# Kernel tuning notes

Measured on AMD Instinct MI355X. Metric: run time of the kernel, lower is better.

## Reference

```python
import jax, jax.numpy as jnp
import numpy as np

B, T, N, D = 4, 24, 5000, 64
M, K = 256, 20
TEMP = 0.5
MASK_T = int(T * 0.2)


def _random_walk(A):
    # D^-1 A with inf -> 0, as in calculate_random_walk_matrix
    deg = A.sum(axis=1)
    d_inv = jnp.where(deg > 0, 1.0 / deg, 0.0)
    return d_inv[:, None] * A


def _gnn(h, S1, S2, W, b):
    # SpatialConvOrderK, order=1, support_len=2, include_self=True
    # h: [B, C, N, T]; diffusion along node axis; 1x1 conv == channel matmul
    m1 = jnp.einsum('bcnt,mn->bcmt', h, S1)
    m2 = jnp.einsum('bcnt,mn->bcmt', h, S2)
    hc = jnp.concatenate([h, m1, m2], axis=1)  # [B, 3C, N, T]
    return jnp.einsum('bcnt,cd->bdnt', hc, W) + b[None, :, None, None]


def _encode(x, S1, S2, W_start, b_start, W1, b1, W2, b2):
    h = x @ W_start + b_start                 # [B, T, N, D]
    h = jnp.transpose(h, (0, 3, 2, 1))        # [B, D, N, T]
    h = jax.nn.relu(_gnn(h, S1, S2, W1, b1))
    h = _gnn(h, S1, S2, W2, b2)
    return h                                  # [B, D, N, T]


def _normalize(z):
    # cosine-similarity normalization over channel axis (dim=1), torch eps=1e-8
    n = jnp.sqrt(jnp.sum(z * z, axis=1, keepdims=True))
    return z / jnp.maximum(n, 1e-8)


def _forward(x, adj, W_start, b_start, W1, b1, W2, b2, Wf1, bf1, Wf2, bf2,
             missing_idx, pos_idx, neg_idx):
    S1 = _random_walk(adj)
    S2 = _random_walk(adj.T)
    h_ori = _encode(x, S1, S2, W_start, b_start, W1, b1, W2, b2)
    # augmented view: time-masked input through the same encoder
    x_aug = x.at[:, :MASK_T].set(0.0)
    h_aug = _encode(x_aug, S1, S2, W_start, b_start, W1, b1, W2, b2)
    # imputation head: final_linear1 -> relu -> final_linear2
    ht = jnp.transpose(h_ori, (0, 3, 2, 1))   # [B, T, N, D]
    y = jax.nn.relu(ht @ Wf1 + bf1) @ Wf2 + bf2  # [B, T, N, 1]
    # vectorized RSCL: batched gather + cosine sim + InfoNCE (label 0 = positive)
    Zo = _normalize(jnp.transpose(h_ori, (0, 1, 3, 2)))  # [B, D, T, N]
    Za = _normalize(jnp.transpose(h_aug, (0, 1, 3, 2)))
    anchor = Zo[..., missing_idx]             # [B, D, T, M]
    pos = Za[..., pos_idx]                    # [B, D, T, M]
    neg = Za[..., neg_idx]                    # [B, D, T, M, K]
    pos_sim = jnp.sum(anchor * pos, axis=1)                  # [B, T, M]
    neg_sim = jnp.einsum('bdtm,bdtmk->btmk', anchor, neg)    # [B, T, M, K]
    logits = jnp.concatenate([pos_sim[..., None], neg_sim], axis=-1) / TEMP
    # cross-entropy with label 0 == logsumexp - positive logit
    loss = jnp.mean(jax.nn.logsumexp(logits, axis=-1) - logits[..., 0])
    return y, loss


def setup_inputs() -> dict:
    key = jax.random.key(0)
    ks = jax.random.split(key, 12)
    x = jax.random.normal(ks[0], (B, T, N, 1), jnp.float32)
    adj = jax.random.uniform(ks[1], (N, N), jnp.float32)
    missing_idx = jax.random.randint(ks[2], (M,), 0, N)
    pos_idx = jax.random.randint(ks[3], (M,), 0, N)
    neg_idx = jax.random.randint(ks[4], (M, K), 0, N)
    s = lambda k, shp, fan: (jax.random.normal(k, shp, jnp.float32) / np.sqrt(fan)).astype(jnp.float32)
    W_start = s(ks[5], (1, D), 1.0)
    b_start = jnp.zeros((D,), jnp.float32)
    W1 = s(ks[6], (3 * D, D), 3.0 * D)
    b1 = jnp.zeros((D,), jnp.float32)
    W2 = s(ks[7], (3 * D, D), 3.0 * D)
    b2 = jnp.zeros((D,), jnp.float32)
    Wf1 = s(ks[8], (D, D // 2), float(D))
    bf1 = jnp.zeros((D // 2,), jnp.float32)
    Wf2 = s(ks[9], (D // 2, 1), float(D // 2))
    bf2 = jnp.zeros((1,), jnp.float32)
    return dict(x=x, adj=adj, W_start=W_start, b_start=b_start, W1=W1, b1=b1,
                W2=W2, b2=b2, Wf1=Wf1, bf1=bf1, Wf2=Wf2, bf2=bf2,
                missing_idx=missing_idx, pos_idx=pos_idx, neg_idx=neg_idx)


def reference(x, adj, W_start, b_start, W1, b1, W2, b2, Wf1, bf1, Wf2, bf2,
              missing_idx, pos_idx, neg_idx):
    return _forward(x, adj, W_start, b_start, W1, b1, W2, b2, Wf1, bf1, Wf2, bf2,
                    missing_idx, pos_idx, neg_idx)
```

## Files before the change

### kernel.cpp

```cpp
#include <hip/hip_runtime.h>

typedef unsigned char u8;
typedef unsigned short u16;
typedef unsigned int u32;
typedef __attribute__((ext_vector_type(8))) short short8;
typedef __attribute__((ext_vector_type(8))) u16 u16x8;
typedef __attribute__((ext_vector_type(4))) float f32x4;
typedef __attribute__((ext_vector_type(4))) int i32x4;
typedef __attribute__((ext_vector_type(8))) int i32x8;

#define N_NODES 5000
#define NP 5120
#define BTOT 96
#define J_DIM 6144
#define TT 24
#define KNEG 20

__device__ __forceinline__ float b2f(u16 u){ union{u32 i; float f;} x; x.i = ((u32)u)<<16; return x.f; }
__device__ __forceinline__ u16 f2b(float f){ union{float fl; u32 i;} x; x.fl = f; u32 r = (x.i + 0x7fffu + ((x.i>>16)&1u))>>16; return (u16)r; }
__device__ __forceinline__ u8 f2e4(float f){ return (u8)(__builtin_amdgcn_cvt_pk_fp8_f32(f, 0.f, 0, false) & 0xff); }

#define GPERM(r) ((((r)>>1)&3) | (((r)&1)<<2))
#define GLOAD16(g, l) __builtin_amdgcn_global_load_lds((const __attribute__((address_space(1))) void*)(g), (__attribute__((address_space(3))) void*)(l), 16, 0, 0)

__global__ void k_prep(const float* __restrict__ Ws, const float* __restrict__ bs,
                       const float* __restrict__ W1, const float* __restrict__ b1,
                       const float* __restrict__ W2, const float* __restrict__ b2,
                       float* __restrict__ consts, u16* __restrict__ w2t)
{
  int d = threadIdx.x;
  float u0=0.f,u1=0.f,u2=0.f,bb=0.f;
  for (int c=0;c<64;c++){
    float w = Ws[c];
    float a = W1[c*64+d], b_ = W1[(64+c)*64+d], cw = W1[(128+c)*64+d];
    u0 += w*a; u1 += w*b_; u2 += w*cw;
    bb += bs[c]*(a+b_+cw);
  }
  bb += b1[d];
  consts[d]=u0; consts[64+d]=u1; consts[128+d]=u2; consts[192+d]=bb;
  __shared__ float rb[64];
  rb[d] = fmaxf(bb, 0.f);
  __syncthreads();
  float cA=0.f,cB=0.f,cC=0.f;
  for (int c=0;c<64;c++){
    float r = rb[c];
    cA += r*W2[c*64+d]; cB += r*W2[(64+c)*64+d]; cC += r*W2[(128+c)*64+d];
  }
  consts[256+d]=cA; consts[320+d]=cB; consts[384+d]=cC;
  for (int c=0;c<192;c++) w2t[d*192 + c] = f2b(W2[c*64 + d]);
  __syncthreads();
  float b2v = b2[d];
  for (int vi=0; vi<4; vi++){
    float vv = cA + ((vi&1) ? cB : 0.f) + ((vi&2) ? cC : 0.f) + b2v;
    rb[d] = vv*vv;
    __syncthreads();
    for (int o=32;o;o>>=1){ if (d<o) rb[d]+=rb[d+o]; __syncthreads(); }
    float nrm = sqrtf(rb[0]);
    consts[448 + vi*64 + d] = vv / fmaxf(nrm, 1e-8f);
    __syncthreads();
  }
}

__global__ __launch_bounds__(256) void k_convT(const float* __restrict__ adj,
    u8* __restrict__ abf, u8* __restrict__ atbf,
    float* __restrict__ degr, float* __restrict__ degc)
{
  __shared__ u8 tN[64][80];
  __shared__ u8 tT[64][80];
  __shared__ float rsum[64];
  __shared__ float cpart[16][64];
  const int tid = threadIdx.x;
  const int bx = blockIdx.x, by = blockIdx.y;
  const int c4 = (tid & 15) * 4;
  const int g  = tid >> 4;
  const int gk = bx*64 + c4;
  float ca0=0.f, ca1=0.f, ca2=0.f, ca3=0.f;
  #pragma unroll
  for (int p=0;p<4;p++){
    int r = p*16 + g;
    int gm = by*64 + r;
    float v0=0.f,v1=0.f,v2=0.f,v3=0.f;
    if (gm < N_NODES && gk + 3 < N_NODES){
      const float4 v = *(const float4*)(adj + (size_t)gm*N_NODES + gk);
      v0=v.x; v1=v.y; v2=v.z; v3=v.w;
    }
    u8 p0=f2e4(v0), p1=f2e4(v1), p2=f2e4(v2), p3=f2e4(v3);
    *(u32*)&tN[r][c4] = (u32)p0 | ((u32)p1<<8) | ((u32)p2<<16) | ((u32)p3<<24);
    tT[c4+0][r]=p0; tT[c4+1][r]=p1; tT[c4+2][r]=p2; tT[c4+3][r]=p3;
    float ls = v0+v1+v2+v3;
    ls += __shfl_xor(ls,1); ls += __shfl_xor(ls,2);
    ls += __shfl_xor(ls,4); ls += __shfl_xor(ls,8);
    if ((tid & 15) == 0) rsum[r] = ls;
    ca0+=v0; ca1+=v1; ca2+=v2; ca3+=v3;
  }
  cpart[g][c4+0]=ca0; cpart[g][c4+1]=ca1; cpart[g][c4+2]=ca2; cpart[g][c4+3]=ca3;
  __syncthreads();
  if (tid < 64){
    int gm = by*64 + tid;
    if (gm < N_NODES && rsum[tid] != 0.f) atomicAdd(&degr[gm], rsum[tid]);
    float cs = 0.f;
    #pragma unroll
    for (int gg=0;gg<16;gg++) cs += cpart[gg][tid];
    int gc = bx*64 + tid;
    if (gc < N_NODES && cs != 0.f) atomicAdd(&degc[gc], cs);
  }
  const int j = tid >> 2, c16 = (tid & 3) * 16;
  *(i32x4*)(abf  + (size_t)(by*64+j)*NP + bx*64 + c16) = *(const i32x4*)(&tN[j][c16]);
  *(i32x4*)(atbf + (size_t)(bx*64+j)*NP + by*64 + c16) = *(const i32x4*)(&tT[j][c16]);
}

__global__ void k_xbf(const float* __restrict__ x, u8* __restrict__ xbf){
  int i4 = (blockIdx.x*256 + threadIdx.x)*4;
  int j = i4 / NP, n = i4 - j*NP;
  u32 w = 0;
  if (j < BTOT){
    #pragma unroll
    for (int e=0;e<4;e++){
      float v = (n+e < N_NODES) ? x[(size_t)j*N_NODES + n + e] : 0.f;
      w |= ((u32)f2e4(v)) << (8*e);
    }
  }
  *(u32*)(xbf + i4) = w;
}

__device__ __forceinline__ i32x8 frag8(const u8* lds, int row, int kb2){
  int g = GPERM(row & 7);
  int ba = row*128 + ((kb2 ^ g)<<4);
  union { i32x8 v; i32x4 h[2]; } f;
  f.h[0] = *(const i32x4*)(lds + ba);
  f.h[1] = *(const i32x4*)(lds + (ba^16));
  return f.v;
}

__global__ __launch_bounds__(256) void k_sgemm8(const u8* __restrict__ abf,
    const u8* __restrict__ atbf, const u8* __restrict__ B,
    float* __restrict__ y1sl, float* __restrict__ y2sl)
{
  __shared__ __align__(16) u8 lA[128*128];
  __shared__ __align__(16) u8 lB[128*128];
  const u8* A = blockIdx.z ? atbf : abf;
  float* ysl = blockIdx.z ? y2sl : y1sl;
  const int tid = threadIdx.x, lane = tid & 63, wv = tid >> 6;
  const int wm = (wv >> 1) * 64, wj = (wv & 1) * 64;
  const int m0 = blockIdx.x * 128;
  const int kbase = blockIdx.y * 640;
  f32x4 acc[4][4] = {};
  const int q = tid >> 3;
  const int sc = ((tid & 7) ^ GPERM(q & 7)) << 4;
  const u8* gA = A + (size_t)(m0 + q)*NP + kbase + sc;
  const u8* gB = B + (size_t)q*NP + kbase + sc;
  for (int k0 = 0; k0 < 640; k0 += 128) {
    #pragma unroll
    for (int s=0;s<4;s++){
      GLOAD16(gA + (size_t)(s*32)*NP + k0, (char*)lA + s*4096 + wv*1024);
      GLOAD16(gB + (size_t)(s*32)*NP + k0, (char*)lB + s*4096 + wv*1024);
    }
    __syncthreads();
    i32x8 af[4], bfv[4];
    const int kb2 = (lane >> 4) * 2;
    #pragma unroll
    for (int i=0;i<4;i++){
      af[i]  = frag8(lA, wm + i*16 + (lane&15), kb2);
      bfv[i] = frag8(lB, wj + i*16 + (lane&15), kb2);
    }
    #pragma unroll
    for (int i=0;i<4;i++)
      #pragma unroll
      for (int j=0;j<4;j++)
        acc[i][j] = __builtin_amdgcn_mfma_scale_f32_16x16x128_f8f6f4(
            af[i], bfv[j], acc[i][j], 0, 0, 0, 0x7f7f7f7f, 0, 0x7f7f7f7f);
    __syncthreads();
  }
  float* yb = ysl + (size_t)blockIdx.y * NP * 128;
  #pragma unroll
  for (int i=0;i<4;i++)
    #pragma unroll
    for (int r=0;r<4;r++){
      int row = m0 + wm + i*16 + (lane>>4)*4 + r;
      #pragma unroll
      for (int j=0;j<4;j++){
        int col = wj + j*16 + (lane&15);
        yb[(size_t)row*128 + col] = acc[i][j][r];
      }
    }
}

__global__ __launch_bounds__(256) void k_yred(const float* __restrict__ y1sl,
    const float* __restrict__ y2sl, const float* __restrict__ degr,
    const float* __restrict__ degc, float* __restrict__ y1r, float* __restrict__ y2r)
{
  __shared__ float tb[128][66];
  const int n0 = blockIdx.x*64;
  const int bt = threadIdx.x & 127, nh = threadIdx.x >> 7;
  const int nl = threadIdx.x & 63, bh = threadIdx.x >> 6;
  #pragma unroll 4
  for (int k=0;k<32;k++){
    int n = nh*32 + k;
    float s = 0.f;
    #pragma unroll
    for (int sl=0; sl<8; sl++) s += y1sl[((size_t)sl*NP + n0+n)*128 + bt];
    tb[bt][n] = s;
  }
  __syncthreads();
  {
    float dv = degr[n0+nl];
    float iv = (dv > 0.f) ? 1.f/dv : 0.f;
    #pragma unroll 4
    for (int b=0;b<32;b++){
      int btw = bh*32 + b;
      y1r[(size_t)btw*NP + n0 + nl] = iv * tb[btw][nl];
    }
  }
  __syncthreads();
  #pragma unroll 4
  for (int k=0;k<32;k++){
    int n = nh*32 + k;
    float s = 0.f;
    #pragma unroll
    for (int sl=0; sl<8; sl++) s += y2sl[((size_t)sl*NP + n0+n)*128 + bt];
    tb[bt][n] = s;
  }
  __syncthreads();
  {
    float dv = degc[n0+nl];
    float iv = (dv > 0.f) ? 1.f/dv : 0.f;
    #pragma unroll 4
    for (int b=0;b<32;b++){
      int btw = bh*32 + b;
      y2r[(size_t)btw*NP + n0 + nl] = iv * tb[btw][nl];
    }
  }
}

__global__ __launch_bounds__(256) void k_h1(const float* __restrict__ x,
    const float* __restrict__ y1r, const float* __restrict__ y2r,
    const float* __restrict__ consts, u8* __restrict__ h1t, u16* __restrict__ h1n)
{
  __shared__ u8 trT[64][80];
  const int tid = threadIdx.x;
  const int n = tid & 63, d0 = (tid >> 6) * 16;
  const int n0 = blockIdx.x * 64;
  const int bt = blockIdx.y;
  const int gn = n0 + n;
  const bool valid = gn < N_NODES;
  float xv  = valid ? x[(size_t)bt*N_NODES + gn] : 0.f;
  float y1s = y1r[(size_t)bt*NP + gn];
  float y2s = y2r[(size_t)bt*NP + gn];
  float hv[16];
  #pragma unroll
  for (int e=0;e<16;e++){
    int d = d0 + e;
    float v = 0.f;
    if (valid)
      v = fmaxf(xv*consts[d] + y1s*consts[64+d] + y2s*consts[128+d] + consts[192+d], 0.f);
    hv[e] = v;
    trT[d][n] = f2e4(v);
  }
  u16x8 p0, p1;
  #pragma unroll
  for (int e=0;e<8;e++){ p0[e]=f2b(hv[e]); p1[e]=f2b(hv[8+e]); }
  u16* dst = h1n + (size_t)gn*J_DIM + bt*64 + d0;
  *(u16x8*)dst = p0;
  *(u16x8*)(dst+8) = p1;
  __syncthreads();
  const int d = tid >> 2, c16 = (tid & 3) * 16;
  *(i32x4*)(h1t + (size_t)(bt*64+d)*NP + n0 + c16) = *(const i32x4*)(&trT[d][c16]);
}

__global__ __launch_bounds__(256) void k_gemm8(
    const u8* __restrict__ abf, const u8* __restrict__ atbf,
    const u8* __restrict__ Bt, u16* __restrict__ Pb, u16* __restrict__ Qb,
    const float* __restrict__ degr, const float* __restrict__ degc)
{
  __shared__ __align__(16) u8 lA[2][16384];
  __shared__ __align__(16) u8 lB[2][16384];
  const u8* A = blockIdx.z ? atbf : abf;
  u16* C = blockIdx.z ? Qb : Pb;
  const float* dg = blockIdx.z ? degc : degr;
  const int tid = threadIdx.x, lane = tid & 63, wv = tid >> 6;
  const int wm = (wv >> 1) * 64, wj = (wv & 1) * 64;
  const int m0 = blockIdx.x * 128;
  const int j0 = blockIdx.y * 128;
  f32x4 acc[4][4] = {};
  const int q = tid >> 3;
  const int sc = ((tid & 7) ^ GPERM(q & 7)) << 4;
  const u8* gA = A + (size_t)(m0 + q)*NP + sc;
  const u8* gB = Bt + (size_t)(j0 + q)*NP + sc;

  #define STAGE8(k0, bufA, bufB) do { \
    _Pragma("unroll") \
    for (int s=0;s<4;s++){ \
      GLOAD16(gA + (size_t)(s*32)*NP + (k0), (char*)(bufA) + s*4096 + wv*1024); \
      GLOAD16(gB + (size_t)(s*32)*NP + (k0), (char*)(bufB) + s*4096 + wv*1024); \
    } \
  } while(0)

  STAGE8(0,   lA[0], lB[0]);
  STAGE8(128, lA[1], lB[1]);
  asm volatile("s_waitcnt vmcnt(8)" ::: "memory");
  __builtin_amdgcn_s_barrier();
  __builtin_amdgcn_sched_barrier(0);

  const int NT = NP/128;
  for (int t = 0; t < NT; t++) {
    const int cur = t & 1;
    const u8* bA = lA[cur];
    const u8* bB = lB[cur];
    i32x8 af[4], bfv[4];
    const int kb2 = (lane >> 4) * 2;
    #pragma unroll
    for (int i=0;i<4;i++){
      af[i]  = frag8(bA, wm + i*16 + (lane&15), kb2);
      bfv[i] = frag8(bB, wj + i*16 + (lane&15), kb2);
    }
    __builtin_amdgcn_s_setprio(1);
    #pragma unroll
    for (int i=0;i<4;i++)
      #pragma unroll
      for (int j=0;j<4;j++)
        acc[i][j] = __builtin_amdgcn_mfma_scale_f32_16x16x128_f8f6f4(
            af[i], bfv[j], acc[i][j], 0, 0, 0, 0x7f7f7f7f, 0, 0x7f7f7f7f);
    __builtin_amdgcn_s_setprio(0);
    __builtin_amdgcn_s_barrier();
    __builtin_amdgcn_sched_barrier(0);
    if (t + 2 < NT) {
      STAGE8((t+2)*128, lA[cur], lB[cur]);
      asm volatile("s_waitcnt vmcnt(8)" ::: "memory");
    } else {
      asm volatile("s_waitcnt vmcnt(0)" ::: "memory");
    }
    __builtin_amdgcn_s_barrier();
    __builtin_amdgcn_sched_barrier(0);
  }
  #undef STAGE8

  #pragma unroll
  for (int i=0;i<4;i++)
    #pragma unroll
    for (int r=0;r<4;r++){
      int row = m0 + wm + i*16 + (lane>>4)*4 + r;
      float dv = dg[row];
      float scl = (dv > 0.f) ? 1.f/dv : 0.f;
      #pragma unroll
      for (int j=0;j<4;j++){
        int col = j0 + wj + j*16 + (lane&15);
        C[(size_t)row*J_DIM + col] = f2b(acc[i][j][r] * scl);
      }
    }
}

__global__ __launch_bounds__(256) void k_comb(const u16* __restrict__ h1n,
  const u16* __restrict__ P, const u16* __restrict__ Q,
  const u16* __restrict__ w2t, const float* __restrict__ b2,
  const float* __restrict__ Wf1, const float* __restrict__ bf1,
  const float* __restrict__ Wf2, const float* __restrict__ bf2,
  u16* __restrict__ horin, float* __restrict__ yout)
{
  __shared__ float w1L[64*33];
  __shared__ float hT[64][65];
  __shared__ float b1L[32], w2Ls[32];
  const int tid = threadIdx.x;
  for (int i = tid; i < 2048; i += 256) w1L[(i>>5)*33 + (i&31)] = Wf1[i];
  if (tid < 32){ b1L[tid] = bf1[tid]; w2Ls[tid] = Wf2[tid]; }
  const int lane = tid & 63;
  const int wv = tid >> 6;
  const int n0 = blockIdx.x * 64 + wv * 16;
  const int bt = blockIdx.y;
  const int rl = lane & 15, kh = lane >> 4;

  f32x4 acc[4] = {};
  const size_t rowoff = (size_t)(n0 + rl) * J_DIM + bt*64;
  const u16* bases[3] = { h1n + rowoff, P + rowoff, Q + rowoff };
  #pragma unroll
  for (int s=0;s<3;s++){
    const u16* base = bases[s];
    #pragma unroll
    for (int kk=0;kk<2;kk++){
      short8 af = *(const short8*)(base + kk*32 + kh*8);
      #pragma unroll
      for (int j=0;j<4;j++){
        short8 bf = *(const short8*)(w2t + (j*16+rl)*192 + s*64 + kk*32 + kh*8);
        acc[j] = __builtin_amdgcn_mfma_f32_16x16x32_bf16(af, bf, acc[j], 0,0,0);
      }
    }
  }
  float hvv[4][4];
  #pragma unroll
  for (int j=0;j<4;j++){
    float bias = b2[j*16 + rl];
    #pragma unroll
    for (int r=0;r<4;r++) hvv[j][r] = acc[j][r] + bias;
  }
  float inv[4];
  #pragma unroll
  for (int r=0;r<4;r++){
    float s = hvv[0][r]*hvv[0][r] + hvv[1][r]*hvv[1][r]
            + hvv[2][r]*hvv[2][r] + hvv[3][r]*hvv[3][r];
    s += __shfl_xor(s,1); s += __shfl_xor(s,2);
    s += __shfl_xor(s,4); s += __shfl_xor(s,8);
    inv[r] = 1.f / fmaxf(sqrtf(s), 1e-8f);
  }
  #pragma unroll
  for (int j=0;j<4;j++){
    int d = j*16 + rl;
    #pragma unroll
    for (int r=0;r<4;r++){
      int nn = n0 + kh*4 + r;
      hT[wv*16 + kh*4 + r][d] = hvv[j][r];
      if (nn < N_NODES)
        horin[((size_t)bt*N_NODES + nn)*64 + d] = f2b(hvv[j][r] * inv[r]);
    }
  }
  __syncthreads();
  const int qd = tid & 3, node = tid >> 2;
  float h[16];
  #pragma unroll
  for (int e=0;e<16;e++) h[e] = hT[node][qd*16 + e];
  float yacc = 0.f;
  #pragma unroll
  for (int jj=0; jj<32; jj++){
    float s = 0.f;
    #pragma unroll
    for (int dl=0; dl<16; dl++) s += h[dl]*w1L[(qd*16+dl)*33 + jj];
    s += __shfl_xor(s, 1);
    s += __shfl_xor(s, 2);
    s += b1L[jj];
    yacc += fmaxf(s, 0.f)*w2Ls[jj];
  }
  int gn = blockIdx.x*64 + node;
  if (qd == 0 && gn < N_NODES)
    yout[(size_t)bt*N_NODES + gn] = yacc + bf2[0];
}

__global__ __launch_bounds__(256) void k_loss(const u16* __restrict__ horin,
  const int* __restrict__ missing, const int* __restrict__ posi, const int* __restrict__ negi,
  const float* __restrict__ degr, const float* __restrict__ degc,
  const float* __restrict__ consts, float* __restrict__ out)
{
  const int lane = threadIdx.x & 63;
  const int wv = threadIdx.x >> 6;
  const int wg = blockIdx.x*4 + wv;
  const int m = wg & 255;
  const int bt = wg >> 8;
  const bool early = (bt % TT) < 4;

  int na = missing[m];
  float va = b2f(horin[((size_t)bt*N_NODES + na)*64 + lane]);

  float lk[KNEG+1];
  #pragma unroll
  for (int k=0;k<=KNEG;k++){
    int node = (k==0) ? posi[m] : negi[m*KNEG + (k-1)];
    float v;
    if (!early) v = b2f(horin[((size_t)bt*N_NODES + node)*64 + lane]);
    else {
      int vi = (degr[node] > 0.f ? 1 : 0) + (degc[node] > 0.f ? 2 : 0);
      v = consts[448 + vi*64 + lane];
    }
    float dp = va*v;
    #pragma unroll
    for (int o=32;o;o>>=1) dp += __shfl_xor(dp, o);
    lk[k] = dp * 2.f;
  }
  float mx = lk[0];
  #pragma unroll
  for (int k=1;k<=KNEG;k++) mx = fmaxf(mx, lk[k]);
  float se = 0.f;
  #pragma unroll
  for (int k=0;k<=KNEG;k++) se += expf(lk[k]-mx);
  float term = logf(se) + mx - lk[0];
  __shared__ float red[4];
  if (lane == 0) red[wv] = term;
  __syncthreads();
  if (threadIdx.x == 0)
    atomicAdd(out + 480000, (red[0]+red[1]+red[2]+red[3]) * (1.f/24576.f));
}

extern "C" void kernel_launch(void* const* d_in, const int* in_sizes, int n_in,
                              void* d_out, int out_size, void* d_ws, size_t ws_size,
                              hipStream_t stream)
{
  const float* x   = (const float*)d_in[0];
  const float* adj = (const float*)d_in[1];
  const float* Ws  = (const float*)d_in[2];
  const float* bs  = (const float*)d_in[3];
  const float* W1  = (const float*)d_in[4];
  const float* b1  = (const float*)d_in[5];
  const float* W2  = (const float*)d_in[6];
  const float* b2  = (const float*)d_in[7];
  const float* Wf1 = (const float*)d_in[8];
  const float* bf1 = (const float*)d_in[9];
  const float* Wf2 = (const float*)d_in[10];
  const float* bf2 = (const float*)d_in[11];
  const int* missing = (const int*)d_in[12];
  const int* posi    = (const int*)d_in[13];
  const int* negi    = (const int*)d_in[14];
  float* out = (float*)d_out;

  char* w = (char*)d_ws;
  u8*  abf   = (u8*) (w + 0);
  u8*  atbf  = (u8*) (w + 26214400);
  u8*  h1t   = (u8*) (w + 52428800);
  u16* h1n   = (u16*)(w + 83886080);
  u16* Pb    = (u16*)(w + 146800640);
  u16* Qb    = (u16*)(w + 209715200);
  u8*  xbf   = (u8*) (w + 272629760);
  float* degr = (float*)(w + 273285120);
  float* degc = (float*)(w + 273305600);
  float* consts = (float*)(w + 273326080);
  u16* w2t   = (u16*)(w + 273330176);
  u16*   horin = (u16*)(w + 0);
  float* y1sl  = (float*)(w + 146800640);
  float* y2sl  = (float*)(w + 167772160);
  float* y1r   = (float*)(w + 209715200);
  float* y2r   = (float*)(w + 212336640);

  hipMemsetAsync(degr, 0, 40960, stream);
  hipMemsetAsync(out + 480000, 0, 4, stream);

  k_prep<<<1, 64, 0, stream>>>(Ws, bs, W1, b1, W2, b2, consts, w2t);
  k_convT<<<dim3(80,80), 256, 0, stream>>>(adj, abf, atbf, degr, degc);
  k_xbf<<<640, 256, 0, stream>>>(x, xbf);
  k_sgemm8<<<dim3(40,8,2), 256, 0, stream>>>(abf, atbf, xbf, y1sl, y2sl);
  k_yred<<<80, 256, 0, stream>>>(y1sl, y2sl, degr, degc, y1r, y2r);
  k_h1<<<dim3(80,96), 256, 0, stream>>>(x, y1r, y2r, consts, h1t, h1n);
  k_gemm8<<<dim3(40,48,2), 256, 0, stream>>>(abf, atbf, h1t, Pb, Qb, degr, degc);
  k_comb<<<dim3(80,96), 256, 0, stream>>>(h1n, Pb, Qb, w2t, b2, Wf1, bf1, Wf2, bf2, horin, out);
  k_loss<<<6144, 256, 0, stream>>>(horin, missing, posi, negi, degr, degc, consts, out);
}
```

Measured before the change: 672.3 us.

## Store diffusion outputs P/Q as fp8 and double-buffer the small fp8 GEMM

```diff
diff --git a/kernel.cpp b/kernel.cpp
--- a/kernel.cpp
+++ b/kernel.cpp
@@ -19,6 +19,23 @@
 __device__ __forceinline__ float b2f(u16 u){ union{u32 i; float f;} x; x.i = ((u32)u)<<16; return x.f; }
 __device__ __forceinline__ u16 f2b(float f){ union{float fl; u32 i;} x; x.fl = f; u32 r = (x.i + 0x7fffu + ((x.i>>16)&1u))>>16; return (u16)r; }
 __device__ __forceinline__ u8 f2e4(float f){ return (u8)(__builtin_amdgcn_cvt_pk_fp8_f32(f, 0.f, 0, false) & 0xff); }
+__device__ __forceinline__ float e4tof(u8 v){
+  u32 s = ((u32)(v & 0x80)) << 24;
+  u32 em = v & 0x7f;
+  union{u32 i; float f;} x;
+  if (em >= 8) x.i = s | ((em + 0x3C0u) << 20);
+  else { x.f = (float)em * 0.001953125f; x.i |= s; }
+  return x.f;
+}
+__device__ __forceinline__ short8 cvt8(u32 w0, u32 w1){
+  short8 r;
+  #pragma unroll
+  for (int e=0;e<4;e++){
+    r[e]   = (short)f2b(e4tof((u8)(w0 >> (8*e))));
+    r[4+e] = (short)f2b(e4tof((u8)(w1 >> (8*e))));
+  }
+  return r;
+}
 
 #define GPERM(r) ((((r)>>1)&3) | (((r)&1)<<2))
 #define GLOAD16(g, l) __builtin_amdgcn_global_load_lds((const __attribute__((address_space(1))) void*)(g), (__attribute__((address_space(3))) void*)(l), 16, 0, 0)
@@ -136,8 +153,8 @@
     const u8* __restrict__ atbf, const u8* __restrict__ B,
     float* __restrict__ y1sl, float* __restrict__ y2sl)
 {
-  __shared__ __align__(16) u8 lA[128*128];
-  __shared__ __align__(16) u8 lB[128*128];
+  __shared__ __align__(16) u8 lA[2][16384];
+  __shared__ __align__(16) u8 lB[2][16384];
   const u8* A = blockIdx.z ? atbf : abf;
   float* ysl = blockIdx.z ? y2sl : y1sl;
   const int tid = threadIdx.x, lane = tid & 63, wv = tid >> 6;
@@ -149,28 +166,53 @@
   const int sc = ((tid & 7) ^ GPERM(q & 7)) << 4;
   const u8* gA = A + (size_t)(m0 + q)*NP + kbase + sc;
   const u8* gB = B + (size_t)q*NP + kbase + sc;
-  for (int k0 = 0; k0 < 640; k0 += 128) {
-    #pragma unroll
-    for (int s=0;s<4;s++){
-      GLOAD16(gA + (size_t)(s*32)*NP + k0, (char*)lA + s*4096 + wv*1024);
-      GLOAD16(gB + (size_t)(s*32)*NP + k0, (char*)lB + s*4096 + wv*1024);
-    }
-    __syncthreads();
+
+  #define SSTAGE8(k0, bufA, bufB) do { \
+    _Pragma("unroll") \
+    for (int s=0;s<4;s++){ \
+      GLOAD16(gA + (size_t)(s*32)*NP + (k0), (char*)(bufA) + s*4096 + wv*1024); \
+      GLOAD16(gB + (size_t)(s*32)*NP + (k0), (char*)(bufB) + s*4096 + wv*1024); \
+    } \
+  } while(0)
+
+  SSTAGE8(0,   lA[0], lB[0]);
+  SSTAGE8(128, lA[1], lB[1]);
+  asm volatile("s_waitcnt vmcnt(8)" ::: "memory");
+  __builtin_amdgcn_s_barrier();
+  __builtin_amdgcn_sched_barrier(0);
+
+  for (int t = 0; t < 5; t++) {
+    const int cur = t & 1;
+    const u8* bA = lA[cur];
+    const u8* bB = lB[cur];
     i32x8 af[4], bfv[4];
     const int kb2 = (lane >> 4) * 2;
     #pragma unroll
     for (int i=0;i<4;i++){
-      af[i]  = frag8(lA, wm + i*16 + (lane&15), kb2);
-      bfv[i] = frag8(lB, wj + i*16 + (lane&15), kb2);
-    }
+      af[i]  = frag8(bA, wm + i*16 + (lane&15), kb2);
+      bfv[i] = frag8(bB, wj + i*16 + (lane&15), kb2);
+    }
+    __builtin_amdgcn_s_setprio(1);
     #pragma unroll
     for (int i=0;i<4;i++)
       #pragma unroll
       for (int j=0;j<4;j++)
         acc[i][j] = __builtin_amdgcn_mfma_scale_f32_16x16x128_f8f6f4(
             af[i], bfv[j], acc[i][j], 0, 0, 0, 0x7f7f7f7f, 0, 0x7f7f7f7f);
-    __syncthreads();
-  }
+    __builtin_amdgcn_s_setprio(0);
+    __builtin_amdgcn_s_barrier();
+    __builtin_amdgcn_sched_barrier(0);
+    if (t + 2 < 5) {
+      SSTAGE8((t+2)*128, lA[cur], lB[cur]);
+      asm volatile("s_waitcnt vmcnt(8)" ::: "memory");
+    } else {
+      asm volatile("s_waitcnt vmcnt(0)" ::: "memory");
+    }
+    __builtin_amdgcn_s_barrier();
+    __builtin_amdgcn_sched_barrier(0);
+  }
+  #undef SSTAGE8
+
   float* yb = ysl + (size_t)blockIdx.y * NP * 128;
   #pragma unroll
   for (int i=0;i<4;i++)
@@ -269,13 +311,13 @@
 
 __global__ __launch_bounds__(256) void k_gemm8(
     const u8* __restrict__ abf, const u8* __restrict__ atbf,
-    const u8* __restrict__ Bt, u16* __restrict__ Pb, u16* __restrict__ Qb,
+    const u8* __restrict__ Bt, u8* __restrict__ Pb, u8* __restrict__ Qb,
     const float* __restrict__ degr, const float* __restrict__ degc)
 {
   __shared__ __align__(16) u8 lA[2][16384];
   __shared__ __align__(16) u8 lB[2][16384];
   const u8* A = blockIdx.z ? atbf : abf;
-  u16* C = blockIdx.z ? Qb : Pb;
+  u8* C = blockIdx.z ? Qb : Pb;
   const float* dg = blockIdx.z ? degc : degr;
   const int tid = threadIdx.x, lane = tid & 63, wv = tid >> 6;
   const int wm = (wv >> 1) * 64, wj = (wv & 1) * 64;
@@ -344,13 +386,13 @@
       #pragma unroll
       for (int j=0;j<4;j++){
         int col = j0 + wj + j*16 + (lane&15);
-        C[(size_t)row*J_DIM + col] = f2b(acc[i][j][r] * scl);
+        C[(size_t)row*J_DIM + col] = f2e4(acc[i][j][r] * scl);
       }
     }
 }
 
 __global__ __launch_bounds__(256) void k_comb(const u16* __restrict__ h1n,
-  const u16* __restrict__ P, const u16* __restrict__ Q,
+  const u8* __restrict__ P8, const u8* __restrict__ Q8,
   const u16* __restrict__ w2t, const float* __restrict__ b2,
   const float* __restrict__ Wf1, const float* __restrict__ bf1,
   const float* __restrict__ Wf2, const float* __restrict__ bf2,
@@ -369,17 +411,31 @@
   const int rl = lane & 15, kh = lane >> 4;
 
   f32x4 acc[4] = {};
-  const size_t rowoff = (size_t)(n0 + rl) * J_DIM + bt*64;
-  const u16* bases[3] = { h1n + rowoff, P + rowoff, Q + rowoff };
-  #pragma unroll
-  for (int s=0;s<3;s++){
-    const u16* base = bases[s];
+  {
+    const u16* base = h1n + (size_t)(n0 + rl)*J_DIM + bt*64;
     #pragma unroll
     for (int kk=0;kk<2;kk++){
       short8 af = *(const short8*)(base + kk*32 + kh*8);
       #pragma unroll
       for (int j=0;j<4;j++){
-        short8 bf = *(const short8*)(w2t + (j*16+rl)*192 + s*64 + kk*32 + kh*8);
+        short8 bf = *(const short8*)(w2t + (j*16+rl)*192 + kk*32 + kh*8);
+        acc[j] = __builtin_amdgcn_mfma_f32_16x16x32_bf16(af, bf, acc[j], 0,0,0);
+      }
+    }
+  }
+  const size_t rowoff8 = (size_t)(n0 + rl) * J_DIM + bt*64;
+  const u8* bases8[2] = { P8 + rowoff8, Q8 + rowoff8 };
+  #pragma unroll
+  for (int s=0;s<2;s++){
+    const u8* base = bases8[s];
+    #pragma unroll
+    for (int kk=0;kk<2;kk++){
+      u32 w0 = *(const u32*)(base + kk*32 + kh*8);
+      u32 w1 = *(const u32*)(base + kk*32 + kh*8 + 4);
+      short8 af = cvt8(w0, w1);
+      #pragma unroll
+      for (int j=0;j<4;j++){
+        short8 bf = *(const short8*)(w2t + (j*16+rl)*192 + (s+1)*64 + kk*32 + kh*8);
         acc[j] = __builtin_amdgcn_mfma_f32_16x16x32_bf16(af, bf, acc[j], 0,0,0);
       }
     }
@@ -502,18 +558,18 @@
   u8*  atbf  = (u8*) (w + 26214400);
   u8*  h1t   = (u8*) (w + 52428800);
   u16* h1n   = (u16*)(w + 83886080);
-  u16* Pb    = (u16*)(w + 146800640);
-  u16* Qb    = (u16*)(w + 209715200);
-  u8*  xbf   = (u8*) (w + 272629760);
-  float* degr = (float*)(w + 273285120);
-  float* degc = (float*)(w + 273305600);
-  float* consts = (float*)(w + 273326080);
-  u16* w2t   = (u16*)(w + 273330176);
-  u16*   horin = (u16*)(w + 0);
-  float* y1sl  = (float*)(w + 146800640);
-  float* y2sl  = (float*)(w + 167772160);
-  float* y1r   = (float*)(w + 209715200);
-  float* y2r   = (float*)(w + 212336640);
+  u8*  Pb    = (u8*) (w + 146800640);
+  u8*  Qb    = (u8*) (w + 178257920);
+  float* y1sl = (float*)(w + 209715200);
+  float* y2sl = (float*)(w + 230686720);
+  float* y1r  = (float*)(w + 251658240);
+  float* y2r  = (float*)(w + 254279680);
+  u8*  xbf   = (u8*) (w + 256901120);
+  float* degr = (float*)(w + 257556480);
+  float* degc = (float*)(w + 257576960);
+  float* consts = (float*)(w + 257597440);
+  u16* w2t   = (u16*)(w + 257601536);
+  u16* horin = (u16*)(w + 0);
 
   hipMemsetAsync(degr, 0, 40960, stream);
   hipMemsetAsync(out + 480000, 0, 4, stream);
```

Result: slower. 691.6 us (+2.9%).

## Enlarge diffusion GEMM tile to 256x256 and double-buffer the slice GEMM

Applied to the files above, without the earlier changes.

```diff
diff --git a/kernel.cpp b/kernel.cpp
--- a/kernel.cpp
+++ b/kernel.cpp
@@ -136,8 +136,8 @@
     const u8* __restrict__ atbf, const u8* __restrict__ B,
     float* __restrict__ y1sl, float* __restrict__ y2sl)
 {
-  __shared__ __align__(16) u8 lA[128*128];
-  __shared__ __align__(16) u8 lB[128*128];
+  __shared__ __align__(16) u8 lA[2][16384];
+  __shared__ __align__(16) u8 lB[2][16384];
   const u8* A = blockIdx.z ? atbf : abf;
   float* ysl = blockIdx.z ? y2sl : y1sl;
   const int tid = threadIdx.x, lane = tid & 63, wv = tid >> 6;
@@ -149,28 +149,53 @@
   const int sc = ((tid & 7) ^ GPERM(q & 7)) << 4;
   const u8* gA = A + (size_t)(m0 + q)*NP + kbase + sc;
   const u8* gB = B + (size_t)q*NP + kbase + sc;
-  for (int k0 = 0; k0 < 640; k0 += 128) {
-    #pragma unroll
-    for (int s=0;s<4;s++){
-      GLOAD16(gA + (size_t)(s*32)*NP + k0, (char*)lA + s*4096 + wv*1024);
-      GLOAD16(gB + (size_t)(s*32)*NP + k0, (char*)lB + s*4096 + wv*1024);
-    }
-    __syncthreads();
+
+  #define SSTAGE8(k0, bufA, bufB) do { \
+    _Pragma("unroll") \
+    for (int s=0;s<4;s++){ \
+      GLOAD16(gA + (size_t)(s*32)*NP + (k0), (char*)(bufA) + s*4096 + wv*1024); \
+      GLOAD16(gB + (size_t)(s*32)*NP + (k0), (char*)(bufB) + s*4096 + wv*1024); \
+    } \
+  } while(0)
+
+  SSTAGE8(0,   lA[0], lB[0]);
+  SSTAGE8(128, lA[1], lB[1]);
+  asm volatile("s_waitcnt vmcnt(8)" ::: "memory");
+  __builtin_amdgcn_s_barrier();
+  __builtin_amdgcn_sched_barrier(0);
+
+  for (int t = 0; t < 5; t++) {
+    const int cur = t & 1;
+    const u8* bA = lA[cur];
+    const u8* bB = lB[cur];
     i32x8 af[4], bfv[4];
     const int kb2 = (lane >> 4) * 2;
     #pragma unroll
     for (int i=0;i<4;i++){
-      af[i]  = frag8(lA, wm + i*16 + (lane&15), kb2);
-      bfv[i] = frag8(lB, wj + i*16 + (lane&15), kb2);
-    }
+      af[i]  = frag8(bA, wm + i*16 + (lane&15), kb2);
+      bfv[i] = frag8(bB, wj + i*16 + (lane&15), kb2);
+    }
+    __builtin_amdgcn_s_setprio(1);
     #pragma unroll
     for (int i=0;i<4;i++)
       #pragma unroll
       for (int j=0;j<4;j++)
         acc[i][j] = __builtin_amdgcn_mfma_scale_f32_16x16x128_f8f6f4(
             af[i], bfv[j], acc[i][j], 0, 0, 0, 0x7f7f7f7f, 0, 0x7f7f7f7f);
-    __syncthreads();
-  }
+    __builtin_amdgcn_s_setprio(0);
+    __builtin_amdgcn_s_barrier();
+    __builtin_amdgcn_sched_barrier(0);
+    if (t + 2 < 5) {
+      SSTAGE8((t+2)*128, lA[cur], lB[cur]);
+      asm volatile("s_waitcnt vmcnt(8)" ::: "memory");
+    } else {
+      asm volatile("s_waitcnt vmcnt(0)" ::: "memory");
+    }
+    __builtin_amdgcn_s_barrier();
+    __builtin_amdgcn_sched_barrier(0);
+  }
+  #undef SSTAGE8
+
   float* yb = ysl + (size_t)blockIdx.y * NP * 128;
   #pragma unroll
   for (int i=0;i<4;i++)
@@ -267,21 +292,22 @@
   *(i32x4*)(h1t + (size_t)(bt*64+d)*NP + n0 + c16) = *(const i32x4*)(&trT[d][c16]);
 }
 
-__global__ __launch_bounds__(256) void k_gemm8(
+__global__ __launch_bounds__(512, 2) void k_gemm8(
     const u8* __restrict__ abf, const u8* __restrict__ atbf,
     const u8* __restrict__ Bt, u16* __restrict__ Pb, u16* __restrict__ Qb,
     const float* __restrict__ degr, const float* __restrict__ degc)
 {
-  __shared__ __align__(16) u8 lA[2][16384];
-  __shared__ __align__(16) u8 lB[2][16384];
+  __shared__ __align__(16) u8 lA[2][32768];
+  __shared__ __align__(16) u8 lB[2][32768];
   const u8* A = blockIdx.z ? atbf : abf;
   u16* C = blockIdx.z ? Qb : Pb;
   const float* dg = blockIdx.z ? degc : degr;
   const int tid = threadIdx.x, lane = tid & 63, wv = tid >> 6;
-  const int wm = (wv >> 1) * 64, wj = (wv & 1) * 64;
-  const int m0 = blockIdx.x * 128;
-  const int j0 = blockIdx.y * 128;
-  f32x4 acc[4][4] = {};
+  const int wm = (wv >> 1) * 64;
+  const int wn = (wv & 1) * 128;
+  const int m0 = blockIdx.x * 256;
+  const int j0 = blockIdx.y * 256;
+  f32x4 acc[4][8] = {};
   const int q = tid >> 3;
   const int sc = ((tid & 7) ^ GPERM(q & 7)) << 4;
   const u8* gA = A + (size_t)(m0 + q)*NP + sc;
@@ -290,8 +316,8 @@
   #define STAGE8(k0, bufA, bufB) do { \
     _Pragma("unroll") \
     for (int s=0;s<4;s++){ \
-      GLOAD16(gA + (size_t)(s*32)*NP + (k0), (char*)(bufA) + s*4096 + wv*1024); \
-      GLOAD16(gB + (size_t)(s*32)*NP + (k0), (char*)(bufB) + s*4096 + wv*1024); \
+      GLOAD16(gA + (size_t)(s*64)*NP + (k0), (char*)(bufA) + s*8192 + wv*1024); \
+      GLOAD16(gB + (size_t)(s*64)*NP + (k0), (char*)(bufB) + s*8192 + wv*1024); \
     } \
   } while(0)
 
@@ -306,20 +332,20 @@
     const int cur = t & 1;
     const u8* bA = lA[cur];
     const u8* bB = lB[cur];
-    i32x8 af[4], bfv[4];
     const int kb2 = (lane >> 4) * 2;
-    #pragma unroll
-    for (int i=0;i<4;i++){
-      af[i]  = frag8(bA, wm + i*16 + (lane&15), kb2);
-      bfv[i] = frag8(bB, wj + i*16 + (lane&15), kb2);
-    }
+    const int rl = lane & 15;
+    i32x8 af[4];
+    #pragma unroll
+    for (int i=0;i<4;i++) af[i] = frag8(bA, wm + i*16 + rl, kb2);
     __builtin_amdgcn_s_setprio(1);
     #pragma unroll
-    for (int i=0;i<4;i++)
+    for (int j=0;j<8;j++){
+      i32x8 bf = frag8(bB, wn + j*16 + rl, kb2);
       #pragma unroll
-      for (int j=0;j<4;j++)
+      for (int i=0;i<4;i++)
         acc[i][j] = __builtin_amdgcn_mfma_scale_f32_16x16x128_f8f6f4(
-            af[i], bfv[j], acc[i][j], 0, 0, 0, 0x7f7f7f7f, 0, 0x7f7f7f7f);
+            af[i], bf, acc[i][j], 0, 0, 0, 0x7f7f7f7f, 0, 0x7f7f7f7f);
+    }
     __builtin_amdgcn_s_setprio(0);
     __builtin_amdgcn_s_barrier();
     __builtin_amdgcn_sched_barrier(0);
@@ -342,8 +368,8 @@
       float dv = dg[row];
       float scl = (dv > 0.f) ? 1.f/dv : 0.f;
       #pragma unroll
-      for (int j=0;j<4;j++){
-        int col = j0 + wj + j*16 + (lane&15);
+      for (int j=0;j<8;j++){
+        int col = j0 + wn + j*16 + (lane&15);
         C[(size_t)row*J_DIM + col] = f2b(acc[i][j][r] * scl);
       }
     }
@@ -524,7 +550,7 @@
   k_sgemm8<<<dim3(40,8,2), 256, 0, stream>>>(abf, atbf, xbf, y1sl, y2sl);
   k_yred<<<80, 256, 0, stream>>>(y1sl, y2sl, degr, degc, y1r, y2r);
   k_h1<<<dim3(80,96), 256, 0, stream>>>(x, y1r, y2r, consts, h1t, h1n);
-  k_gemm8<<<dim3(40,48,2), 256, 0, stream>>>(abf, atbf, h1t, Pb, Qb, degr, degc);
+  k_gemm8<<<dim3(20,24,2), 512, 0, stream>>>(abf, atbf, h1t, Pb, Qb, degr, degc);
   k_comb<<<dim3(80,96), 256, 0, stream>>>(h1n, Pb, Qb, w2t, b2, Wf1, bf1, Wf2, bf2, horin, out);
   k_loss<<<6144, 256, 0, stream>>>(horin, missing, posi, negi, degr, degc, consts, out);
 }
```

Result: no change. 683.5 us (+1.7%).
